# Kernel tuning notes

Measured on AMD Instinct MI355X. Metric: run time of the kernel, lower is better.

## Reference

```python
import jax, jax.numpy as jnp
import numpy as np

NUM_HEADS = 12
HEAD_DIM = 64
EPS = 1e-5


def _ln(t, g, b):
    m = t.mean(-1, keepdims=True)
    v = ((t - m) ** 2).mean(-1, keepdims=True)
    return (t - m) * jax.lax.rsqrt(v + EPS) * g + b


def _pool(t, conv_w, g, b, B, H, W, C):
    # t: [B, heads, 1+H*W, C] -> depthwise-conv pooled [B, heads, 1+Hp*Wp, C]
    cls = t[:, :, :1, :]
    sp = t[:, :, 1:, :].reshape(B * NUM_HEADS, H, W, C).transpose(0, 3, 1, 2)
    y = jax.lax.conv_general_dilated(
        sp, conv_w, (2, 2), [(1, 1), (1, 1)],
        feature_group_count=C,
        dimension_numbers=('NCHW', 'OIHW', 'NCHW'))
    Hp, Wp = y.shape[2], y.shape[3]
    y = y.reshape(B, NUM_HEADS, C, Hp * Wp).transpose(0, 1, 3, 2)
    y = jnp.concatenate([cls, y], axis=2)
    return _ln(y, g, b), (Hp, Wp)


def _rel_dist(q_s, k_s):
    q_ratio = max(k_s / q_s, 1.0)
    k_ratio = max(q_s / k_s, 1.0)
    d = jnp.arange(q_s)[:, None] * q_ratio - jnp.arange(k_s)[None, :] * k_ratio
    d = d + (k_s - 1) * k_ratio
    return d.astype(jnp.int32)


def _forward(x, pool_q_w, pool_k_w, pool_v_w,
             norm_q_g, norm_q_b, norm_k_g, norm_k_b, norm_v_g, norm_v_b,
             wq, bq, wk, bk, wv, bv, proj_w, proj_b,
             rel_pos_h, rel_pos_w, feat_h, feat_w):
    B, N, D = x.shape
    C = D // NUM_HEADS
    t = x.reshape(B, N, NUM_HEADS, C).transpose(0, 2, 1, 3)  # [B,h,N,C]
    q, (qh, qw) = _pool(t, pool_q_w, norm_q_g, norm_q_b, B, feat_h, feat_w, C)
    k, (kh, kw) = _pool(t, pool_k_w, norm_k_g, norm_k_b, B, feat_h, feat_w, C)
    v, _ = _pool(t, pool_v_w, norm_v_g, norm_v_b, B, feat_h, feat_w, C)

    def proj_heads(y, w, bias):
        n = y.shape[2]
        y = y.transpose(0, 2, 1, 3).reshape(B, n, D)
        y = y @ w + bias
        return y.reshape(B, n, NUM_HEADS, HEAD_DIM).transpose(0, 2, 1, 3)

    q = proj_heads(q, wq, bq)
    k = proj_heads(k, wk, bk)
    v = proj_heads(v, wv, bv)

    scale = HEAD_DIM ** -0.5
    attn = jnp.einsum('bhqd,bhkd->bhqk', q * scale, k)

    # spatial relative position bias (cal_rel_pos_type), cls token excluded
    Rh = rel_pos_h[_rel_dist(qh, kh)]   # [qh,kh,hd]
    Rw = rel_pos_w[_rel_dist(qw, kw)]   # [qw,kw,hd]
    r_q = q[:, :, 1:, :].reshape(B, NUM_HEADS, qh, qw, HEAD_DIM)
    rel_h = jnp.einsum('byhwc,hkc->byhwk', r_q, Rh)
    rel_w = jnp.einsum('byhwc,wkc->byhwk', r_q, Rw)
    bias2d = (rel_h[..., :, None] + rel_w[..., None, :]).reshape(
        B, NUM_HEADS, qh * qw, kh * kw)
    attn = attn.at[:, :, 1:, 1:].add(bias2d)

    attn = jax.nn.softmax(attn, axis=-1)
    out = jnp.einsum('bhqk,bhkd->bhqd', attn, v)
    out = out + q  # residual pooling
    out = out.transpose(0, 2, 1, 3).reshape(B, -1, NUM_HEADS * HEAD_DIM)
    return out @ proj_w + proj_b


def setup_inputs() -> dict:
    key = jax.random.key(0)
    ks = jax.random.split(key, 16)
    B, D, C = 16, 768, 64
    H = W = 56
    N = H * W + 1
    rs = 2 * 28 - 1
    rnd = lambda i, sh, s: jax.random.normal(ks[i], sh, jnp.float32) * s
    return {
        'x': rnd(0, (B, N, D), 1.0),
        'pool_q_w': rnd(1, (C, 1, 3, 3), 0.1),
        'pool_k_w': rnd(2, (C, 1, 3, 3), 0.1),
        'pool_v_w': rnd(3, (C, 1, 3, 3), 0.1),
        'norm_q_g': jnp.ones((C,), jnp.float32),
        'norm_q_b': jnp.zeros((C,), jnp.float32),
        'norm_k_g': jnp.ones((C,), jnp.float32),
        'norm_k_b': jnp.zeros((C,), jnp.float32),
        'norm_v_g': jnp.ones((C,), jnp.float32),
        'norm_v_b': jnp.zeros((C,), jnp.float32),
        'wq': rnd(4, (D, D), 0.02), 'bq': jnp.zeros((D,), jnp.float32),
        'wk': rnd(5, (D, D), 0.02), 'bk': jnp.zeros((D,), jnp.float32),
        'wv': rnd(6, (D, D), 0.02), 'bv': jnp.zeros((D,), jnp.float32),
        'proj_w': rnd(7, (D, D), 0.02), 'proj_b': jnp.zeros((D,), jnp.float32),
        'rel_pos_h': rnd(8, (rs, HEAD_DIM), 0.02),
        'rel_pos_w': rnd(9, (rs, HEAD_DIM), 0.02),
        'feat_h': 56, 'feat_w': 56,
    }


def reference(x, pool_q_w, pool_k_w, pool_v_w,
              norm_q_g, norm_q_b, norm_k_g, norm_k_b, norm_v_g, norm_v_b,
              wq, bq, wk, bk, wv, bv, proj_w, proj_b,
              rel_pos_h, rel_pos_w, feat_h, feat_w):
    return _forward(x, pool_q_w, pool_k_w, pool_v_w,
                    norm_q_g, norm_q_b, norm_k_g, norm_k_b,
                    norm_v_g, norm_v_b,
                    wq, bq, wk, bk, wv, bv, proj_w, proj_b,
                    rel_pos_h, rel_pos_w, int(feat_h), int(feat_w))
```

## Files before the change

kernel.cpp:

```cpp
#include <hip/hip_runtime.h>
#include <stdint.h>

#define NUM_HEADS 12
#define HEAD_DIM  64
#define HWDIM     56
#define PHDIM     28
#define NTOK      785
#define NIN       3137
#define BATCH     16
#define DMODEL    768
#define BHCNT     192
#define LOG2E     1.44269504f

typedef __attribute__((ext_vector_type(8))) short bf16x8;
typedef __attribute__((ext_vector_type(4))) short s16x4;
typedef __attribute__((ext_vector_type(4))) float f32x4;

static __device__ __forceinline__ float bf2f(short s) {
  unsigned u = ((unsigned)(unsigned short)s) << 16;
  float f; __builtin_memcpy(&f, &u, 4); return f;
}
static __device__ __forceinline__ short f2bf(float f) {
  unsigned u; __builtin_memcpy(&u, &f, 4);
  unsigned r = u + 0x7FFFu + ((u >> 16) & 1u);
  return (short)(r >> 16);
}
static __device__ __forceinline__ float fexp2(float x) {
#if defined(__has_builtin)
#if __has_builtin(__builtin_amdgcn_exp2f)
  return __builtin_amdgcn_exp2f(x);
#else
  return exp2f(x);
#endif
#else
  return exp2f(x);
#endif
}

static __device__ __forceinline__ int xcd_chunk(int orig, int nwg) {
  int xcd = orig & 7;
  int within = orig >> 3;
  int q = nwg >> 3, r = nwg & 7;
  int base = (xcd < r) ? xcd * (q + 1) : r * (q + 1) + (xcd - r) * q;
  return base + within;
}

#if defined(__has_builtin)
#if __has_builtin(__builtin_amdgcn_global_load_lds)
#define HAVE_GLLDS 1
#endif
#endif

static __device__ __forceinline__ void gl_lds16(const short* g, short* l) {
#ifdef HAVE_GLLDS
  __builtin_amdgcn_global_load_lds(
      (const __attribute__((address_space(1))) void*)g,
      (__attribute__((address_space(3))) void*)l, 16, 0, 0);
#else
  int lane = threadIdx.x & 63;
  *(bf16x8*)(l + lane * 8) = *(const bf16x8*)g;
#endif
}

__global__ __launch_bounds__(192) void pool_ln_kernel(
    const float* __restrict__ x,
    const float* __restrict__ wq9, const float* __restrict__ wk9, const float* __restrict__ wv9,
    const float* __restrict__ gq, const float* __restrict__ bq,
    const float* __restrict__ gk, const float* __restrict__ bk,
    const float* __restrict__ gv, const float* __restrict__ bv,
    short* __restrict__ Pq, short* __restrict__ Pk, short* __restrict__ Pv)
{
  __shared__ __align__(16) float wt_s[3][9][64];
  int tid = threadIdx.x;
  int blk = xcd_chunk(blockIdx.x, 16 * 197);
  int b = blk / 197;
  int n0 = (blk - b * 197) * 4;

  for (int idx = tid; idx < 3 * 576; idx += 192) {
    int conv = idx / 576, rem = idx - conv * 576;
    int c = rem / 9, tap = rem - c * 9;
    const float* wsrc = (conv == 0) ? wq9 : (conv == 1) ? wk9 : wv9;
    wt_s[conv][tap][c] = wsrc[c * 9 + tap];
  }
  __syncthreads();

  int ch0 = tid * 4;
  int c4 = ch0 & 63;
  f32x4 g_q = *(const f32x4*)&gq[c4], b_q = *(const f32x4*)&bq[c4];
  f32x4 g_k = *(const f32x4*)&gk[c4], b_k = *(const f32x4*)&bk[c4];
  f32x4 g_v = *(const f32x4*)&gv[c4], b_v = *(const f32x4*)&bv[c4];

  for (int tt = 0; tt < 4; ++tt) {
    int n = n0 + tt;
    if (n >= NTOK) break;
    f32x4 aq = (f32x4){0.f, 0.f, 0.f, 0.f}, ak = aq, av = aq;
    if (n == 0) {
      f32x4 x4 = *(const f32x4*)&x[((size_t)b * NIN) * DMODEL + ch0];
      aq = ak = av = x4;
    } else {
      int s = n - 1;
      int i = s / PHDIM, j = s - i * PHDIM;
#pragma unroll
      for (int di = 0; di < 3; ++di) {
        int ii = 2 * i - 1 + di;
        if (ii < 0 || ii >= HWDIM) continue;
#pragma unroll
        for (int dj = 0; dj < 3; ++dj) {
          int jj = 2 * j - 1 + dj;
          if (jj < 0 || jj >= HWDIM) continue;
          f32x4 x4 = *(const f32x4*)&x[((size_t)b * NIN + 1 + ii * HWDIM + jj) * DMODEL + ch0];
          int tap = di * 3 + dj;
          f32x4 w0 = *(const f32x4*)&wt_s[0][tap][c4];
          f32x4 w1 = *(const f32x4*)&wt_s[1][tap][c4];
          f32x4 w2 = *(const f32x4*)&wt_s[2][tap][c4];
          aq += w0 * x4; ak += w1 * x4; av += w2 * x4;
        }
      }
    }
    size_t obase = ((size_t)b * NTOK + n) * DMODEL + ch0;
    {
      float sm = aq[0] + aq[1] + aq[2] + aq[3];
#pragma unroll
      for (int m = 1; m < 16; m <<= 1) sm += __shfl_xor(sm, m);
      float mn = sm * (1.f / 64.f);
      f32x4 d = aq - mn;
      float vs = d[0]*d[0] + d[1]*d[1] + d[2]*d[2] + d[3]*d[3];
#pragma unroll
      for (int m = 1; m < 16; m <<= 1) vs += __shfl_xor(vs, m);
      float rs = rsqrtf(vs * (1.f / 64.f) + 1e-5f);
      s16x4 o;
#pragma unroll
      for (int e = 0; e < 4; ++e) o[e] = f2bf(d[e] * rs * g_q[e] + b_q[e]);
      *(s16x4*)&Pq[obase] = o;
    }
    {
      float sm = ak[0] + ak[1] + ak[2] + ak[3];
#pragma unroll
      for (int m = 1; m < 16; m <<= 1) sm += __shfl_xor(sm, m);
      float mn = sm * (1.f / 64.f);
      f32x4 d = ak - mn;
      float vs = d[0]*d[0] + d[1]*d[1] + d[2]*d[2] + d[3]*d[3];
#pragma unroll
      for (int m = 1; m < 16; m <<= 1) vs += __shfl_xor(vs, m);
      float rs = rsqrtf(vs * (1.f / 64.f) + 1e-5f);
      s16x4 o;
#pragma unroll
      for (int e = 0; e < 4; ++e) o[e] = f2bf(d[e] * rs * g_k[e] + b_k[e]);
      *(s16x4*)&Pk[obase] = o;
    }
    {
      float sm = av[0] + av[1] + av[2] + av[3];
#pragma unroll
      for (int m = 1; m < 16; m <<= 1) sm += __shfl_xor(sm, m);
      float mn = sm * (1.f / 64.f);
      f32x4 d = av - mn;
      float vs = d[0]*d[0] + d[1]*d[1] + d[2]*d[2] + d[3]*d[3];
#pragma unroll
      for (int m = 1; m < 16; m <<= 1) vs += __shfl_xor(vs, m);
      float rs = rsqrtf(vs * (1.f / 64.f) + 1e-5f);
      s16x4 o;
#pragma unroll
      for (int e = 0; e < 4; ++e) o[e] = f2bf(d[e] * rs * g_v[e] + b_v[e]);
      *(s16x4*)&Pv[obase] = o;
    }
  }
}

__global__ __launch_bounds__(256) void trans_kernel(
    const float* __restrict__ s0, const float* __restrict__ s1,
    const float* __restrict__ s2, const float* __restrict__ s3,
    short* __restrict__ d0, short* __restrict__ d1,
    short* __restrict__ d2, short* __restrict__ d3)
{
  __shared__ float tile[32][33];
  int z = blockIdx.z;
  const float* s = (z == 0) ? s0 : (z == 1) ? s1 : (z == 2) ? s2 : s3;
  short* d = (z == 0) ? d0 : (z == 1) ? d1 : (z == 2) ? d2 : d3;
  int k0 = blockIdx.x * 32, n0 = blockIdx.y * 32;
  int tx = threadIdx.x, ty = threadIdx.y;
#pragma unroll
  for (int jj = 0; jj < 4; ++jj)
    tile[ty + jj * 8][tx] = s[(size_t)(k0 + ty + jj * 8) * DMODEL + n0 + tx];
  __syncthreads();
#pragma unroll
  for (int jj = 0; jj < 4; ++jj)
    d[(size_t)(n0 + ty + jj * 8) * DMODEL + k0 + tx] = f2bf(tile[tx][ty + jj * 8]);
}

static __device__ __forceinline__ void gemm_core(
    short* As, short* Bs,
    const short* __restrict__ A, const short* __restrict__ Bt,
    const float* __restrict__ bias, void* __restrict__ outp, void* __restrict__ outp2,
    int rowbase, int colbase, int M, int Nn, int mode)
{
  const int K = DMODEL;
  int tid = threadIdx.x;
  int wid = tid >> 6, lane = tid & 63;
  int lg = lane >> 4, lq = lane & 15;
  int wm = wid >> 1, wn = wid & 1;

  f32x4 acc[4][2];
#pragma unroll
  for (int i = 0; i < 4; ++i)
#pragma unroll
    for (int j = 0; j < 2; ++j) acc[i][j] = (f32x4){0.f, 0.f, 0.f, 0.f};

  const short* AgP[2];
  const short* BgP;
  {
#pragma unroll
    for (int m = 0; m < 2; ++m) {
      int ch = m * 256 + tid;
      int row = ch >> 2, j = ch & 3;
      int gcol = (j ^ (row & 3)) << 3;
      int ar = min(rowbase + row, M - 1);
      AgP[m] = A + (size_t)ar * K + gcol;
    }
    int ch = tid;
    int row = ch >> 2, j = ch & 3;
    int gcol = (j ^ (row & 3)) << 3;
    int br = min(colbase + row, Nn - 1);
    BgP = Bt + (size_t)br * K + gcol;
  }

  auto stage = [&](int kt, int buf) __attribute__((always_inline)) {
    short* Ab = As + buf * 4096;
    short* Bb = Bs + buf * 2048;
#pragma unroll
    for (int m = 0; m < 2; ++m)
      gl_lds16(AgP[m] + kt, Ab + m * 2048 + wid * 512);
    gl_lds16(BgP + kt, Bb + wid * 512);
  };

  stage(0, 0);
  __syncthreads();
  int cur = 0;
  for (int kt = 0; kt < K; kt += 32) {
    if (kt + 32 < K) stage(kt + 32, cur ^ 1);
    const short* Ac = As + cur * 4096;
    const short* Bc = Bs + cur * 2048;
    bf16x8 aFrag[4], bFrag[2];
#pragma unroll
    for (int mi = 0; mi < 4; ++mi) {
      int r = wm * 64 + mi * 16 + lq;
      int slot = lg ^ (r & 3);
      aFrag[mi] = *(const bf16x8*)&Ac[r * 32 + slot * 8];
    }
#pragma unroll
    for (int ni = 0; ni < 2; ++ni) {
      int r = wn * 32 + ni * 16 + lq;
      int slot = lg ^ (r & 3);
      bFrag[ni] = *(const bf16x8*)&Bc[r * 32 + slot * 8];
    }
    __builtin_amdgcn_s_setprio(1);
#pragma unroll
    for (int mi = 0; mi < 4; ++mi)
#pragma unroll
      for (int ni = 0; ni < 2; ++ni)
        acc[mi][ni] = __builtin_amdgcn_mfma_f32_16x16x32_bf16(aFrag[mi], bFrag[ni], acc[mi][ni], 0, 0, 0);
    __builtin_amdgcn_s_setprio(0);
    __syncthreads();
    cur ^= 1;
  }

  if (mode >= 3) {
    int myhead = colbase >> 6;
#pragma unroll
    for (int mi = 0; mi < 4; ++mi) {
      int rowq = rowbase + wm * 64 + mi * 16 + lg * 4;
#pragma unroll
      for (int r = 0; r < 4; ++r) {
        int row = rowq + r;
        if (row < M) {
          int bb = row / NTOK, nn = row - bb * NTOK;
          size_t abase = ((size_t)(bb * NUM_HEADS + myhead) * NTOK + nn) * 128;
#pragma unroll
          for (int ni = 0; ni < 2; ++ni) {
            int col = colbase + wn * 32 + ni * 16 + lq;
            int c = col & 63;
            float v = acc[mi][ni][r] + bias[col];
            ((short*)outp2)[abase + c] = f2bf(v);
          }
        }
      }
    }
    if (colbase == 0) {
      int rz = rowbase + wm * 64 + lane;
      if (rz < M) {
        int bb = rz / NTOK, nn = rz - bb * NTOK;
        short* dst = (short*)outp2 + ((size_t)(bb * NUM_HEADS + myhead) * NTOK + nn) * 128 + 64;
        if (mode == 3) {
          bf16x8 z = {0, 0, 0, 0, 0, 0, 0, 0};
#pragma unroll
          for (int zc = 0; zc < 8; ++zc) *(bf16x8*)(dst + zc * 8) = z;
        } else {
          int ki = -100, kj = -100;
          if (nn >= 1) { int km1 = nn - 1; ki = km1 / PHDIM; kj = km1 - ki * PHDIM; }
#pragma unroll
          for (int zc = 0; zc < 8; ++zc) {
            bf16x8 o = {0, 0, 0, 0, 0, 0, 0, 0};
#pragma unroll
            for (int e = 0; e < 8; ++e) {
              int d = 64 + zc * 8 + e;
              if (d == 64 + ki || d == 92 + kj) o[e] = (short)0x3F80;
            }
            *(bf16x8*)(dst + zc * 8) = o;
          }
        }
      }
    }
    return;
  }

#pragma unroll
  for (int mi = 0; mi < 4; ++mi) {
    int rowq = rowbase + wm * 64 + mi * 16 + lg * 4;
#pragma unroll
    for (int r = 0; r < 4; ++r) {
      int row = rowq + r;
      if (row < M) {
        if (mode == 2) {
          float bb = bias[row];
#pragma unroll
          for (int ni = 0; ni < 2; ++ni) {
            int col = colbase + wn * 32 + ni * 16 + lq;
            if (col < Nn) {
              int b = col / NTOK, n = col - b * NTOK;
              float v = acc[mi][ni][r] + bb;
              ((short*)outp)[((size_t)b * DMODEL + row) * NTOK + n] = f2bf(v);
            }
          }
        } else {
#pragma unroll
          for (int ni = 0; ni < 2; ++ni) {
            int col = colbase + wn * 32 + ni * 16 + lq;
            float v = acc[mi][ni][r] + bias[col];
            ((float*)outp)[(size_t)row * DMODEL + col] = v;
          }
        }
      }
    }
  }
}

__global__ __launch_bounds__(256, 3) void gemm_qkv_kernel(
    const short* __restrict__ Pq, const short* __restrict__ WqT,
    const float* __restrict__ bq, short* __restrict__ qaug,
    const short* __restrict__ Pk, const short* __restrict__ WkT,
    const float* __restrict__ bk, short* __restrict__ kaug,
    const short* __restrict__ WvT, const short* __restrict__ Pv,
    const float* __restrict__ bv, short* __restrict__ vtg)
{
  __shared__ short As[2 * 4096];
  __shared__ short Bs[2 * 2048];
  const int NWG = 3558;
  int lid = xcd_chunk(blockIdx.x, NWG);
  if (lid < 2376) {
    int which = lid / 1188;
    int sub = lid - which * 1188;
    int rowbase = (sub / 12) * 128;
    int colbase = (sub % 12) * 64;
    if (which == 0)
      gemm_core(As, Bs, Pq, WqT, bq, nullptr, (void*)qaug,
                rowbase, colbase, BATCH * NTOK, DMODEL, 3);
    else
      gemm_core(As, Bs, Pk, WkT, bk, nullptr, (void*)kaug,
                rowbase, colbase, BATCH * NTOK, DMODEL, 4);
  } else {
    int sub = lid - 2376;
    int rowbase = (sub % 6) * 128;
    int colbase = (sub / 6) * 64;
    gemm_core(As, Bs, WvT, Pv, bv, (void*)vtg, nullptr,
              rowbase, colbase, DMODEL, BATCH * NTOK, 2);
  }
}

__global__ __launch_bounds__(256, 3) void gemm_proj_kernel(
    const short* __restrict__ Afin, const short* __restrict__ WpT,
    const float* __restrict__ bp, float* __restrict__ outp)
{
  __shared__ short As[2 * 4096];
  __shared__ short Bs[2 * 2048];
  const int NWG = 1188;
  int lid = xcd_chunk(blockIdx.x, NWG);
  int rowbase = (lid / 12) * 128;
  int colbase = (lid % 12) * 64;
  gemm_core(As, Bs, Afin, WpT, bp, (void*)outp, nullptr,
            rowbase, colbase, BATCH * NTOK, DMODEL, 0);
}

__global__ __launch_bounds__(256) void relbias_kernel(
    const short* __restrict__ qaug_in, const float* __restrict__ rph,
    const float* __restrict__ rpw, short* __restrict__ qaug)
{
  int line = blockIdx.x;
  int bh = blockIdx.y;
  int mode = blockIdx.z;
  __shared__ __align__(16) float qt_s[28 * 68];
  __shared__ __align__(16) float rt_s[28 * 68];
  int tid = threadIdx.x;
  const float* rp = (mode == 0) ? rph : rpw;
  for (int idx = tid; idx < 28 * 64; idx += 256) {
    int rr = idx >> 6, c = idx & 63;
    int qi = (mode == 0) ? (1 + line * PHDIM + rr) : (1 + rr * PHDIM + line);
    qt_s[rr * 68 + c] = bf2f(qaug_in[((size_t)bh * NTOK + qi) * 128 + c]);
    rt_s[rr * 68 + c] = rp[(line - rr + 27) * HEAD_DIM + c];
  }
  __syncthreads();
  for (int o = tid; o < 784; o += 256) {
    int kk = o / PHDIM, rr = o - kk * PHDIM;
    const f32x4* qa = (const f32x4*)&qt_s[rr * 68];
    const f32x4* ra = (const f32x4*)&rt_s[kk * 68];
    f32x4 a4 = (f32x4){0.f, 0.f, 0.f, 0.f};
#pragma unroll
    for (int i = 0; i < 16; ++i) a4 += qa[i] * ra[i];
    float s = (a4[0] + a4[1] + a4[2] + a4[3]) * 8.0f;
    int qi = (mode == 0) ? (1 + line * PHDIM + rr) : (1 + rr * PHDIM + line);
    int dim = (mode == 0) ? (64 + kk) : (92 + kk);
    qaug[((size_t)bh * NTOK + qi) * 128 + dim] = f2bf(s);
  }
}

__global__ __launch_bounds__(256) void flash7_kernel(
    const short* __restrict__ qaug, const short* __restrict__ kaug,
    const short* __restrict__ vtg, short* __restrict__ Afin)
{
  int id = blockIdx.x;
  int slot = id >> 3;
  int bh = (id & 7) * 24 + slot / 13;
  int qt = slot - (slot / 13) * 13;
  int qbase = qt * 64;
  int tid = threadIdx.x, wid = tid >> 6, lane = tid & 63;
  int lg = lane >> 4, lq = lane & 15;

  __shared__ __align__(16) short ks[64 * 128];
  __shared__ __align__(16) short vt[64 * 64];
  __shared__ __align__(16) float axl[4][16];

  int qi0 = qbase + wid * 16 + lq;
  int qiq = min(qi0, NTOK - 1);
  const short* qrow = qaug + ((size_t)bh * NTOK + qiq) * 128;
  bf16x8 bq[4];
#pragma unroll
  for (int c = 0; c < 4; ++c) bq[c] = *(const bf16x8*)(qrow + c * 32 + lg * 8);

  float m_l = -3e30f, l_l = 0.f;
  f32x4 acc[4];
#pragma unroll
  for (int ch = 0; ch < 4; ++ch) acc[ch] = (f32x4){0.f, 0.f, 0.f, 0.f};

  const float s2 = 0.125f * LOG2E;
  const short* kbase = kaug + (size_t)bh * NTOK * 128;
  const short* vbase = vtg + (size_t)bh * (size_t)HEAD_DIM * NTOK;

  int koffK[4], kslot[4];
#pragma unroll
  for (int m = 0; m < 4; ++m) {
    int c = m * 256 + tid;
    int rr = c >> 4, j = c & 15;
    koffK[m] = ((rr & 15) >> 2) * 16 + (rr >> 4) * 4 + (rr & 3);
    kslot[m] = (j ^ (rr & 15)) << 3;
  }
  int c0 = tid, c1 = 256 + tid;
  int vr0 = c0 >> 3, vj0 = c0 & 7;
  int vr1 = c1 >> 3, vj1 = c1 & 7;
  const short* vsrc0 = vbase + (size_t)vr0 * NTOK + ((vj0 ^ (vr0 & 7)) << 3);
  const short* vsrc1 = vbase + (size_t)vr1 * NTOK + ((vj1 ^ (vr1 & 7)) << 3);

  auto step_body = [&](int kvb, bool last) __attribute__((always_inline)) {
    __syncthreads();
#pragma unroll
    for (int m = 0; m < 4; ++m)
      gl_lds16(kbase + (size_t)min(kvb + koffK[m], NTOK - 1) * 128 + kslot[m],
               ks + m * 2048 + wid * 512);
    gl_lds16(vsrc0 + kvb, vt + wid * 512);
    gl_lds16(vsrc1 + kvb, vt + 2048 + wid * 512);
    __syncthreads();

    float p[16];
#pragma unroll
    for (int kt = 0; kt < 4; ++kt) {
      int kl = kt * 16 + lq;
      const char* kp = (const char*)ks + kl * 256;
      int swz = kl & 15;
      f32x4 s = (f32x4){0.f, 0.f, 0.f, 0.f};
      __builtin_amdgcn_s_setprio(1);
#pragma unroll
      for (int c = 0; c < 4; ++c) {
        bf16x8 aK = *(const bf16x8*)(kp + (((c * 4 + lg) ^ swz) << 4));
        s = __builtin_amdgcn_mfma_f32_16x16x32_bf16(aK, bq[c], s, 0, 0, 0);
      }
      __builtin_amdgcn_s_setprio(0);
#pragma unroll
      for (int r = 0; r < 4; ++r) {
        int i = kt * 4 + r;
        float v = s[r] * s2;
        if (last) {
          int key = kvb + 16 * lg + i;
          if (key >= NTOK) v = -3e30f;
        }
        p[i] = v;
      }
    }

    float pm = p[0];
#pragma unroll
    for (int i = 1; i < 16; ++i) pm = fmaxf(pm, p[i]);
    pm = fmaxf(pm, __shfl_xor(pm, 16));
    pm = fmaxf(pm, __shfl_xor(pm, 32));
    if (!__all(pm - m_l <= 11.5f)) {
      float mnew = fmaxf(m_l, pm);
      float alpha = fexp2(m_l - mnew);
      m_l = mnew;
      l_l *= alpha;
      if (lg == 0) axl[wid][lq] = alpha;
      f32x4 av = *(const f32x4*)&axl[wid][lg * 4];
#pragma unroll
      for (int ch = 0; ch < 4; ++ch)
#pragma unroll
        for (int r = 0; r < 4; ++r) acc[ch][r] *= av[r];
    }
    float ps = 0.f;
#pragma unroll
    for (int i = 0; i < 16; ++i) { p[i] = fexp2(p[i] - m_l); ps += p[i]; }
    ps += __shfl_xor(ps, 16);
    ps += __shfl_xor(ps, 32);
    l_l += ps;

    bf16x8 pa0, pa1;
#pragma unroll
    for (int j = 0; j < 4; ++j) {
      unsigned u0, u1, v0, v1;
      __builtin_memcpy(&u0, &p[2 * j], 4);
      __builtin_memcpy(&u1, &p[2 * j + 1], 4);
      __builtin_memcpy(&v0, &p[8 + 2 * j], 4);
      __builtin_memcpy(&v1, &p[8 + 2 * j + 1], 4);
      ((unsigned*)&pa0)[j] = (u0 >> 16) | (u1 & 0xFFFF0000u);
      ((unsigned*)&pa1)[j] = (v0 >> 16) | (v1 & 0xFFFF0000u);
    }
    __builtin_amdgcn_s_setprio(1);
#pragma unroll
    for (int ch = 0; ch < 4; ++ch) {
      int d = ch * 16 + lq;
      const char* vrow = (const char*)vt + d * 128;
      int swz = lq & 7;
      bf16x8 bv0 = *(const bf16x8*)(vrow + (((2 * lg + 0) ^ swz) << 4));
      bf16x8 bv1 = *(const bf16x8*)(vrow + (((2 * lg + 1) ^ swz) << 4));
      acc[ch] = __builtin_amdgcn_mfma_f32_16x16x32_bf16(pa0, bv0, acc[ch], 0, 0, 0);
      acc[ch] = __builtin_amdgcn_mfma_f32_16x16x32_bf16(pa1, bv1, acc[ch], 0, 0, 0);
    }
    __builtin_amdgcn_s_setprio(0);
  };

  for (int step = 0; step < 12; ++step) step_body(step * 64, false);
  step_body(12 * 64, true);

  if (lg == 0) axl[wid][lq] = l_l;
  f32x4 lv = *(const f32x4*)&axl[wid][lg * 4];
  int b = bh / NUM_HEADS, h = bh - b * NUM_HEADS;
#pragma unroll
  for (int r = 0; r < 4; ++r) {
    int qi = qbase + wid * 16 + lg * 4 + r;
    if (qi < NTOK) {
      float inv = 1.f / lv[r];
#pragma unroll
      for (int ch = 0; ch < 4; ++ch) {
        int d = ch * 16 + lq;
        float o = acc[ch][r] * inv + bf2f(qaug[((size_t)bh * NTOK + qi) * 128 + d]);
        Afin[((size_t)b * NTOK + qi) * DMODEL + h * HEAD_DIM + d] = f2bf(o);
      }
    }
  }
}

extern "C" void kernel_launch(void* const* d_in, const int* in_sizes, int n_in,
                              void* d_out, int out_size, void* d_ws, size_t ws_size,
                              hipStream_t stream)
{
  (void)in_sizes; (void)n_in; (void)out_size; (void)ws_size;
  const float* x   = (const float*)d_in[0];
  const float* pqw = (const float*)d_in[1];
  const float* pkw = (const float*)d_in[2];
  const float* pvw = (const float*)d_in[3];
  const float* gq  = (const float*)d_in[4];
  const float* bq_ = (const float*)d_in[5];
  const float* gk  = (const float*)d_in[6];
  const float* bk_ = (const float*)d_in[7];
  const float* gv  = (const float*)d_in[8];
  const float* bv_ = (const float*)d_in[9];
  const float* wq  = (const float*)d_in[10];
  const float* bqp = (const float*)d_in[11];
  const float* wk  = (const float*)d_in[12];
  const float* bkp = (const float*)d_in[13];
  const float* wv  = (const float*)d_in[14];
  const float* bvp = (const float*)d_in[15];
  const float* wp  = (const float*)d_in[16];
  const float* bpp = (const float*)d_in[17];
  const float* rph = (const float*)d_in[18];
  const float* rpw = (const float*)d_in[19];

  char* ws = (char*)d_ws;
  size_t off = 0;
  auto alloc = [&](size_t bytes) -> void* {
    void* p = ws + off; off += (bytes + 255) & ~(size_t)255; return p;
  };
  const size_t MROWS = (size_t)BATCH * NTOK;
  short* Pq  = (short*)alloc(MROWS * DMODEL * 2);
  short* Pk  = (short*)alloc(MROWS * DMODEL * 2);
  short* Pv  = (short*)alloc(MROWS * DMODEL * 2);
  short* WqT = (short*)alloc((size_t)DMODEL * DMODEL * 2);
  short* WkT = (short*)alloc((size_t)DMODEL * DMODEL * 2);
  short* WvT = (short*)alloc((size_t)DMODEL * DMODEL * 2);
  short* WpT = (short*)alloc((size_t)DMODEL * DMODEL * 2);
  short* vtg = (short*)alloc(MROWS * DMODEL * 2 + 8192);
  short* qaug = (short*)alloc((size_t)BHCNT * NTOK * 128 * 2 + 8192);
  short* kaug = (short*)alloc((size_t)BHCNT * NTOK * 128 * 2 + 8192);
  short* Afin = (short*)alloc(MROWS * DMODEL * 2);

  pool_ln_kernel<<<dim3(16 * 197), 192, 0, stream>>>(
      x, pqw, pkw, pvw, gq, bq_, gk, bk_, gv, bv_, Pq, Pk, Pv);
  trans_kernel<<<dim3(24, 24, 4), dim3(32, 8), 0, stream>>>(
      wq, wk, wv, wp, WqT, WkT, WvT, WpT);
  gemm_qkv_kernel<<<dim3(3558), 256, 0, stream>>>(
      Pq, WqT, bqp, qaug, Pk, WkT, bkp, kaug, WvT, Pv, bvp, vtg);
  relbias_kernel<<<dim3(28, BHCNT, 2), 256, 0, stream>>>(qaug, rph, rpw, qaug);
  flash7_kernel<<<dim3(2496), 256, 0, stream>>>(qaug, kaug, vtg, Afin);
  gemm_proj_kernel<<<dim3(1188), 256, 0, stream>>>(Afin, WpT, bpp, (float*)d_out);
}
```

Baseline: 357.6 us.

## Process two 64-row query tiles per block in flash attention

Each flash-attention block now handles 128 query rows as two independent 64-row sub-tiles that share every K/V tile loaded into LDS. This halves the global K/V traffic and barrier count per query row, and the grid shrinks from 2496 to 1344 blocks. In exchange, register use roughly doubles (two accumulator sets and Q fragments), which may lower occupancy. Tail padding also grows slightly, since 785 rows no longer split into 128-row tiles as tightly.

```diff
diff --git a/kernel.cpp b/kernel.cpp
--- a/kernel.cpp
+++ b/kernel.cpp
@@ -421,15 +421,15 @@
   }
 }
 
-__global__ __launch_bounds__(256) void flash7_kernel(
+__global__ __launch_bounds__(256) void flash8_kernel(
     const short* __restrict__ qaug, const short* __restrict__ kaug,
     const short* __restrict__ vtg, short* __restrict__ Afin)
 {
   int id = blockIdx.x;
   int slot = id >> 3;
-  int bh = (id & 7) * 24 + slot / 13;
-  int qt = slot - (slot / 13) * 13;
-  int qbase = qt * 64;
+  int bh = (id & 7) * 24 + slot / 7;
+  int qt = slot - (slot / 7) * 7;
+  int qbase = qt * 128;
   int tid = threadIdx.x, wid = tid >> 6, lane = tid & 63;
   int lg = lane >> 4, lq = lane & 15;
 
@@ -437,17 +437,23 @@
   __shared__ __align__(16) short vt[64 * 64];
   __shared__ __align__(16) float axl[4][16];
 
-  int qi0 = qbase + wid * 16 + lq;
-  int qiq = min(qi0, NTOK - 1);
-  const short* qrow = qaug + ((size_t)bh * NTOK + qiq) * 128;
-  bf16x8 bq[4];
-#pragma unroll
-  for (int c = 0; c < 4; ++c) bq[c] = *(const bf16x8*)(qrow + c * 32 + lg * 8);
-
-  float m_l = -3e30f, l_l = 0.f;
-  f32x4 acc[4];
-#pragma unroll
-  for (int ch = 0; ch < 4; ++ch) acc[ch] = (f32x4){0.f, 0.f, 0.f, 0.f};
+  const short* qb = qaug + (size_t)bh * NTOK * 128;
+  int qiA = min(qbase + wid * 16 + lq, NTOK - 1);
+  int qiB = min(qbase + 64 + wid * 16 + lq, NTOK - 1);
+  bf16x8 bqA[4], bqB[4];
+#pragma unroll
+  for (int c = 0; c < 4; ++c) {
+    bqA[c] = *(const bf16x8*)(qb + (size_t)qiA * 128 + c * 32 + lg * 8);
+    bqB[c] = *(const bf16x8*)(qb + (size_t)qiB * 128 + c * 32 + lg * 8);
+  }
+
+  float mA = -3e30f, lA = 0.f, mB = -3e30f, lB = 0.f;
+  f32x4 accA[4], accB[4];
+#pragma unroll
+  for (int ch = 0; ch < 4; ++ch) {
+    accA[ch] = (f32x4){0.f, 0.f, 0.f, 0.f};
+    accB[ch] = (f32x4){0.f, 0.f, 0.f, 0.f};
+  }
 
   const float s2 = 0.125f * LOG2E;
   const short* kbase = kaug + (size_t)bh * NTOK * 128;
@@ -467,16 +473,8 @@
   const short* vsrc0 = vbase + (size_t)vr0 * NTOK + ((vj0 ^ (vr0 & 7)) << 3);
   const short* vsrc1 = vbase + (size_t)vr1 * NTOK + ((vj1 ^ (vr1 & 7)) << 3);
 
-  auto step_body = [&](int kvb, bool last) __attribute__((always_inline)) {
-    __syncthreads();
-#pragma unroll
-    for (int m = 0; m < 4; ++m)
-      gl_lds16(kbase + (size_t)min(kvb + koffK[m], NTOK - 1) * 128 + kslot[m],
-               ks + m * 2048 + wid * 512);
-    gl_lds16(vsrc0 + kvb, vt + wid * 512);
-    gl_lds16(vsrc1 + kvb, vt + 2048 + wid * 512);
-    __syncthreads();
-
+  auto tile_pass = [&](const bf16x8* bq, float& m_l, float& l_l, f32x4* acc,
+                       int kvb, bool last) __attribute__((always_inline)) {
     float p[16];
 #pragma unroll
     for (int kt = 0; kt < 4; ++kt) {
@@ -552,22 +550,54 @@
     __builtin_amdgcn_s_setprio(0);
   };
 
+  auto step_body = [&](int kvb, bool last) __attribute__((always_inline)) {
+    __syncthreads();
+#pragma unroll
+    for (int m = 0; m < 4; ++m)
+      gl_lds16(kbase + (size_t)min(kvb + koffK[m], NTOK - 1) * 128 + kslot[m],
+               ks + m * 2048 + wid * 512);
+    gl_lds16(vsrc0 + kvb, vt + wid * 512);
+    gl_lds16(vsrc1 + kvb, vt + 2048 + wid * 512);
+    __syncthreads();
+    tile_pass(bqA, mA, lA, accA, kvb, last);
+    tile_pass(bqB, mB, lB, accB, kvb, last);
+  };
+
   for (int step = 0; step < 12; ++step) step_body(step * 64, false);
   step_body(12 * 64, true);
 
-  if (lg == 0) axl[wid][lq] = l_l;
-  f32x4 lv = *(const f32x4*)&axl[wid][lg * 4];
   int b = bh / NUM_HEADS, h = bh - b * NUM_HEADS;
-#pragma unroll
-  for (int r = 0; r < 4; ++r) {
-    int qi = qbase + wid * 16 + lg * 4 + r;
-    if (qi < NTOK) {
-      float inv = 1.f / lv[r];
-#pragma unroll
-      for (int ch = 0; ch < 4; ++ch) {
-        int d = ch * 16 + lq;
-        float o = acc[ch][r] * inv + bf2f(qaug[((size_t)bh * NTOK + qi) * 128 + d]);
-        Afin[((size_t)b * NTOK + qi) * DMODEL + h * HEAD_DIM + d] = f2bf(o);
+  if (lg == 0) axl[wid][lq] = lA;
+  {
+    f32x4 lv = *(const f32x4*)&axl[wid][lg * 4];
+#pragma unroll
+    for (int r = 0; r < 4; ++r) {
+      int qi = qbase + wid * 16 + lg * 4 + r;
+      if (qi < NTOK) {
+        float inv = 1.f / lv[r];
+#pragma unroll
+        for (int ch = 0; ch < 4; ++ch) {
+          int d = ch * 16 + lq;
+          float o = accA[ch][r] * inv + bf2f(qb[(size_t)qi * 128 + d]);
+          Afin[((size_t)b * NTOK + qi) * DMODEL + h * HEAD_DIM + d] = f2bf(o);
+        }
+      }
+    }
+  }
+  if (lg == 0) axl[wid][lq] = lB;
+  {
+    f32x4 lv = *(const f32x4*)&axl[wid][lg * 4];
+#pragma unroll
+    for (int r = 0; r < 4; ++r) {
+      int qi = qbase + 64 + wid * 16 + lg * 4 + r;
+      if (qi < NTOK) {
+        float inv = 1.f / lv[r];
+#pragma unroll
+        for (int ch = 0; ch < 4; ++ch) {
+          int d = ch * 16 + lq;
+          float o = accB[ch][r] * inv + bf2f(qb[(size_t)qi * 128 + d]);
+          Afin[((size_t)b * NTOK + qi) * DMODEL + h * HEAD_DIM + d] = f2bf(o);
+        }
       }
     }
   }
@@ -624,6 +654,6 @@
   gemm_qkv_kernel<<<dim3(3558), 256, 0, stream>>>(
       Pq, WqT, bqp, qaug, Pk, WkT, bkp, kaug, WvT, Pv, bvp, vtg);
   relbias_kernel<<<dim3(28, BHCNT, 2), 256, 0, stream>>>(qaug, rph, rpw, qaug);
-  flash7_kernel<<<dim3(2496), 256, 0, stream>>>(qaug, kaug, vtg, Afin);
+  flash8_kernel<<<dim3(1344), 256, 0, stream>>>(qaug, kaug, vtg, Afin);
   gemm_proj_kernel<<<dim3(1188), 256, 0, stream>>>(Afin, WpT, bpp, (float*)d_out);
 }
```

Measured after the change: 389.9 us. 9.0% more time.
